# Kernel optimization log

Hardware: AMD Instinct MI355X
Metric: run time of the kernel (lower is better)

## Reference

```python
import jax, jax.numpy as jnp
import numpy as np

N, V, E, C_IN, C_OUT = 4, 4096, 2048, 64, 64


def setup_inputs() -> dict:
    key = jax.random.key(0)
    k_x, k_h, k_th = jax.random.split(key, 3)
    x = jax.random.normal(k_x, (N, V, C_IN), dtype=jnp.float32)
    H = (jax.random.uniform(k_h, (N, V, E)) < 0.05).astype(jnp.float32)
    # guarantee every vertex and every hyperedge has degree >= 1 (code divides by degree)
    v_idx = jnp.arange(V)
    H = H.at[:, v_idx, v_idx % E].set(1.0)
    # xavier_uniform for theta
    limit = float(np.sqrt(6.0 / (C_IN + C_OUT)))
    theta = jax.random.uniform(k_th, (C_IN, C_OUT), minval=-limit, maxval=limit, dtype=jnp.float32)
    bias = jnp.zeros((C_OUT,), dtype=jnp.float32)
    return {"x": x, "H": H, "theta": theta, "bias": bias}


def reference(x, H, theta, bias):
    # x: [N,V,C], H: [N,V,E] incidence, theta: [C,O], bias: [O]
    # Original builds diag_embed(1/deg) and multiplies; equivalent to direct
    # per-row / per-column scaling of H (same math, no NxVxV / NxExE diagonals).
    dv = 1.0 / H.sum(-1)            # [N,V] vertex degrees
    de = 1.0 / H.sum(1)             # [N,E] hyperedge degrees
    y = jnp.einsum('nvc,co->nvo', x, theta)          # [N,V,O]
    HDe = H * de[:, None, :]                          # H @ De  -> [N,V,E]
    y = jnp.einsum('nvc,nve->nec', y, HDe)            # vertex -> edge  [N,E,O]
    HDv = H * dv[:, :, None]                          # Dv @ H -> [N,V,E]
    y = jnp.einsum('nec,nve->nvc', y, HDv)            # edge -> vertex  [N,V,O]
    return y + bias[None, None, :]
```

## Files before the change

kernel.cpp:

```cpp
#include <hip/hip_runtime.h>
#include <hip/hip_bf16.h>
#include <stdint.h>

#define N_B 4
#define NV 4096
#define NE 2048

typedef float    f32x4  __attribute__((ext_vector_type(4)));
typedef __bf16   bf16x8 __attribute__((ext_vector_type(8)));
typedef unsigned short u16;
typedef u16      u16x8  __attribute__((ext_vector_type(8)));
typedef uint32_t u32x4  __attribute__((ext_vector_type(4)));

__device__ __forceinline__ u16 f2bf_rne(float f) {
    uint32_t u = __builtin_bit_cast(uint32_t, f);
    u += 0x7FFFu + ((u >> 16) & 1u);
    return (u16)(u >> 16);
}
__device__ __forceinline__ float bf2f(u16 h) {
    uint32_t u = ((uint32_t)h) << 16;
    return __builtin_bit_cast(float, u);
}
__device__ __forceinline__ f32x4 mfma_bf16(u16x8 a, u16x8 b, f32x4 c) {
    return __builtin_amdgcn_mfma_f32_16x16x32_bf16(
        __builtin_bit_cast(bf16x8, a), __builtin_bit_cast(bf16x8, b), c, 0, 0, 0);
}
__device__ __forceinline__ u16x8 expand8(uint32_t byte) {
    u32x4 w;
#pragma unroll
    for (int p = 0; p < 4; ++p) {
        const uint32_t lo = (byte >> (2 * p)) & 1u;
        const uint32_t hi = (byte >> (2 * p + 1)) & 1u;
        w[p] = (lo | (hi << 16)) * 0x3F80u;
    }
    return __builtin_bit_cast(u16x8, w);
}

__global__ __launch_bounds__(256) void k_pack(const float* __restrict__ H,
                                              uint32_t* __restrict__ HB,
                                              uint32_t* __restrict__ HT) {
    __shared__ float tile[64][65];
    const int bid = blockIdx.x;
    const int ex = bid & 31, vy = (bid >> 5) & 63, n = bid >> 11;
    const int e0 = ex * 64, v0 = vy * 64;
    const int t = threadIdx.x;
    const float* __restrict__ Hn = H + ((size_t)n * NV + v0) * NE + e0;

#pragma unroll
    for (int i = 0; i < 4; ++i) {
        const int idx = i * 256 + t;
        const int row = idx >> 4;
        const int q = (idx & 15) * 4;
        const float4 hv = *(const float4*)(Hn + (size_t)row * NE + q);
        tile[row][q] = hv.x; tile[row][q + 1] = hv.y;
        tile[row][q + 2] = hv.z; tile[row][q + 3] = hv.w;
    }
    __syncthreads();

    if (t < 128) {
        const int v = t >> 1, we = t & 1;
        uint32_t u = 0;
#pragma unroll
        for (int j = 0; j < 32; ++j)
            u |= (tile[v][we * 32 + j] != 0.0f) ? (1u << j) : 0u;
        HB[(((size_t)n * (NV / 16) + ((v0 + v) >> 4)) * (NE / 32) + (e0 >> 5) + we) * 16 +
           ((v0 + v) & 15)] = u;
    } else {
        const int e = (t - 128) >> 1, wv = t & 1;
        uint32_t u = 0;
#pragma unroll
        for (int j = 0; j < 32; ++j)
            u |= (tile[wv * 32 + j][e] != 0.0f) ? (1u << j) : 0u;
        HT[(((size_t)n * (NE / 16) + ((e0 + e) >> 4)) * (NV / 32) + (v0 >> 5) + wv) * 16 +
           ((e0 + e) & 15)] = u;
    }
}

__global__ __launch_bounds__(256) void k_xtheta(const float* __restrict__ x,
                                                const float* __restrict__ th,
                                                u16* __restrict__ Yh,
                                                u16* __restrict__ Yl) {
    __shared__ float xs[64][65];
    __shared__ float ts[64][65];
    const int t = threadIdx.x;
    const int n  = blockIdx.x >> 6;
    const int v0 = (blockIdx.x & 63) * 64;

#pragma unroll
    for (int i = 0; i < 4; ++i) {
        const int idx = i * 256 + t;
        const int row = idx >> 4, q = (idx & 15) * 4;
        const float4 xv = *(const float4*)&x[((size_t)(n * NV + v0 + row)) * 64 + q];
        const float4 tv = *(const float4*)&th[(size_t)row * 64 + q];
        xs[row][q] = xv.x; xs[row][q + 1] = xv.y; xs[row][q + 2] = xv.z; xs[row][q + 3] = xv.w;
        ts[row][q] = tv.x; ts[row][q + 1] = tv.y; ts[row][q + 2] = tv.z; ts[row][q + 3] = tv.w;
    }
    __syncthreads();

    const int v4 = (t & 15) * 4;
    const int c4 = (t >> 4) * 4;
    float acc[4][4] = {};
#pragma unroll
    for (int k = 0; k < 64; ++k) {
        float tv[4], xv[4];
#pragma unroll
        for (int i = 0; i < 4; ++i) { tv[i] = ts[k][c4 + i]; xv[i] = xs[v4 + i][k]; }
#pragma unroll
        for (int i = 0; i < 4; ++i)
#pragma unroll
            for (int j = 0; j < 4; ++j) acc[i][j] += tv[i] * xv[j];
    }
#pragma unroll
    for (int i = 0; i < 4; ++i) {
        ushort4 hi, lo;
        u16 h;
        h = f2bf_rne(acc[i][0]); hi.x = h; lo.x = f2bf_rne(acc[i][0] - bf2f(h));
        h = f2bf_rne(acc[i][1]); hi.y = h; lo.y = f2bf_rne(acc[i][1] - bf2f(h));
        h = f2bf_rne(acc[i][2]); hi.z = h; lo.z = f2bf_rne(acc[i][2] - bf2f(h));
        h = f2bf_rne(acc[i][3]); hi.w = h; lo.w = f2bf_rne(acc[i][3] - bf2f(h));
        const size_t o = ((size_t)n * 64 + c4 + i) * NV + v0 + v4;
        *(ushort4*)&Yh[o] = hi;
        *(ushort4*)&Yl[o] = lo;
    }
}

__global__ __launch_bounds__(256, 8) void k_v2e(const uint32_t* __restrict__ HT,
                                                const uint32_t* __restrict__ HB,
                                                const u16* __restrict__ Yh,
                                                const u16* __restrict__ Yl,
                                                float* __restrict__ P2,
                                                float* __restrict__ de,
                                                float* __restrict__ dv) {
    const int t = threadIdx.x;
    const int s2 = gridDim.y;
    const int lin = blockIdx.x + 32 * (blockIdx.y + s2 * blockIdx.z);
    const int nb = 32 * s2 * N_B;

    if (t < 64) {
        const int total = N_B * NE + N_B * NV;
        for (int id = lin * 64 + t; id < total; id += nb * 64) {
            if (id < N_B * NE) {
                const int n_ = id >> 11, e = id & (NE - 1);
                const uint32_t* p =
                    HT + ((size_t)n_ * (NE / 16) + (e >> 4)) * ((NV / 32) * 16) + (e & 15);
                uint32_t s = 0;
#pragma unroll 4
                for (int wv = 0; wv < NV / 32; ++wv) s += __popc(p[(size_t)wv * 16]);
                de[id] = (float)s;
            } else {
                const int j = id - N_B * NE;
                const int n_ = j >> 12, v = j & (NV - 1);
                const uint32_t* p =
                    HB + ((size_t)n_ * (NV / 16) + (v >> 4)) * ((NE / 32) * 16) + (v & 15);
                uint32_t s = 0;
#pragma unroll 4
                for (int we = 0; we < NE / 32; ++we) s += __popc(p[(size_t)we * 16]);
                dv[j] = (float)s;
            }
        }
    }

    const int wid = (lin & 7) * (nb >> 3) + (lin >> 3);
    const int n   = wid / (32 * s2);
    const int rem = wid % (32 * s2);
    const int sp  = rem >> 5;
    const int e0  = (rem & 31) * 64;

    const int krange = NV / s2;
    const int kk0 = sp * krange;
    const int S   = krange / 32;

    const int w = t >> 6, l = t & 63;
    const int lq = l >> 4, lr = l & 15;
    const int sh = lq * 8;
    const int hstride = (NV / 32) * 16;

    const uint32_t* __restrict__ ht =
        HT + ((size_t)n * (NE / 16) + (e0 >> 4)) * hstride + (kk0 >> 5) * 16 + lr;
    const u16* __restrict__ ybh = Yh + ((size_t)n * 64 + w * 16 + lr) * NV + kk0 + lq * 8;
    const u16* __restrict__ ybl = Yl + ((size_t)n * 64 + w * 16 + lr) * NV + kk0 + lq * 8;

    f32x4 acc0 = {0.f,0.f,0.f,0.f}, acc1 = acc0, acc2 = acc0, acc3 = acc0;

    uint32_t A[2][4];
#pragma unroll
    for (int d = 0; d < 2; ++d) {
        A[d][0] = ht[0 * hstride + d * 16];
        A[d][1] = ht[1 * hstride + d * 16];
        A[d][2] = ht[2 * hstride + d * 16];
        A[d][3] = ht[3 * hstride + d * 16];
    }
    u16x8 BH[2], BL[2];
    BH[0] = *(const u16x8*)ybh;
    BL[0] = *(const u16x8*)ybl;

#define V2E_STEP(s, u, GA, GB)                                                \
    {                                                                         \
        const uint32_t a0 = A[u][0], a1 = A[u][1], a2 = A[u][2], a3 = A[u][3];\
        if (GA) {                                                             \
            A[u][0] = ht[0 * hstride + ((s) + 2) * 16];                       \
            A[u][1] = ht[1 * hstride + ((s) + 2) * 16];                       \
            A[u][2] = ht[2 * hstride + ((s) + 2) * 16];                       \
            A[u][3] = ht[3 * hstride + ((s) + 2) * 16];                       \
        }                                                                     \
        if (GB) {                                                             \
            BH[((u) + 1) & 1] = *(const u16x8*)(ybh + ((s) + 1) * 32);        \
            BL[((u) + 1) & 1] = *(const u16x8*)(ybl + ((s) + 1) * 32);        \
        }                                                                     \
        const u16x8 bh = BH[u], bl = BL[u];                                   \
        u16x8 a;                                                              \
        a = expand8((a0 >> sh) & 0xFF);                                       \
        acc0 = mfma_bf16(a, bh, acc0); acc0 = mfma_bf16(a, bl, acc0);         \
        a = expand8((a1 >> sh) & 0xFF);                                       \
        acc1 = mfma_bf16(a, bh, acc1); acc1 = mfma_bf16(a, bl, acc1);         \
        a = expand8((a2 >> sh) & 0xFF);                                       \
        acc2 = mfma_bf16(a, bh, acc2); acc2 = mfma_bf16(a, bl, acc2);         \
        a = expand8((a3 >> sh) & 0xFF);                                       \
        acc3 = mfma_bf16(a, bh, acc3); acc3 = mfma_bf16(a, bl, acc3);         \
    }

    int sb = 0;
    for (; sb < S - 2; sb += 2) {
        V2E_STEP(sb + 0, 0, true, true)
        V2E_STEP(sb + 1, 1, true, true)
    }
    V2E_STEP(sb + 0, 0, false, true)
    V2E_STEP(sb + 1, 1, false, false)
#undef V2E_STEP

    float* pb = P2 + (((size_t)sp * N_B + n) * 64 + w * 16 + lr) * NE + e0 + lq * 4;
    *(f32x4*)(pb + 0)  = acc0;
    *(f32x4*)(pb + 16) = acc1;
    *(f32x4*)(pb + 32) = acc2;
    *(f32x4*)(pb + 48) = acc3;
}

__global__ __launch_bounds__(256) void k_red2(const float* __restrict__ P2,
                                              const float* __restrict__ de,
                                              u16* __restrict__ Zh,
                                              u16* __restrict__ Zl, int nsp) {
    const int i = blockIdx.x * 256 + threadIdx.x;
    const int row = i >> 9;
    const int e4  = (i & 511) * 4;
    const int n   = row >> 6;

    float4 a = make_float4(0.f, 0.f, 0.f, 0.f);
    for (int sp = 0; sp < nsp; ++sp) {
        const float4 p = *(const float4*)&P2[((size_t)sp * 256 + row) * NE + e4];
        a.x += p.x; a.y += p.y; a.z += p.z; a.w += p.w;
    }
    const float4 d = *(const float4*)&de[(size_t)n * NE + e4];
    float z[4] = {a.x / d.x, a.y / d.y, a.z / d.z, a.w / d.w};
    ushort4 hi, lo;
    u16 h;
    h = f2bf_rne(z[0]); hi.x = h; lo.x = f2bf_rne(z[0] - bf2f(h));
    h = f2bf_rne(z[1]); hi.y = h; lo.y = f2bf_rne(z[1] - bf2f(h));
    h = f2bf_rne(z[2]); hi.z = h; lo.z = f2bf_rne(z[2] - bf2f(h));
    h = f2bf_rne(z[3]); hi.w = h; lo.w = f2bf_rne(z[3] - bf2f(h));
    *(ushort4*)&Zh[(size_t)row * NE + e4] = hi;
    *(ushort4*)&Zl[(size_t)row * NE + e4] = lo;
}

__global__ __launch_bounds__(256, 8) void k_e2v(const uint32_t* __restrict__ HB,
                                                const u16* __restrict__ Zh,
                                                const u16* __restrict__ Zl,
                                                float* __restrict__ P3) {
    const int t = threadIdx.x;
    const int s3 = gridDim.y;
    const int lin = blockIdx.x + 64 * (blockIdx.y + s3 * blockIdx.z);
    const int nb = 64 * s3 * N_B;

    const int wid = (lin & 7) * (nb >> 3) + (lin >> 3);
    const int n   = wid / (64 * s3);
    const int rem = wid % (64 * s3);
    const int sp  = rem >> 6;
    const int v0  = (rem & 63) * 64;

    const int krange = NE / s3;
    const int kk0 = sp * krange;
    const int S   = krange / 32;

    const int w = t >> 6, l = t & 63;
    const int lq = l >> 4, lr = l & 15;
    const int sh = lq * 8;
    const int estride = (NE / 32) * 16;

    const uint32_t* __restrict__ hb =
        HB + ((size_t)n * (NV / 16) + (v0 >> 4)) * estride + (kk0 >> 5) * 16 + lr;
    const u16* __restrict__ zbh = Zh + ((size_t)n * 64 + w * 16 + lr) * NE + kk0 + lq * 8;
    const u16* __restrict__ zbl = Zl + ((size_t)n * 64 + w * 16 + lr) * NE + kk0 + lq * 8;

    f32x4 acc0 = {0.f,0.f,0.f,0.f}, acc1 = acc0, acc2 = acc0, acc3 = acc0;

    uint32_t A[2][4];
#pragma unroll
    for (int d = 0; d < 2; ++d) {
        A[d][0] = hb[0 * estride + d * 16];
        A[d][1] = hb[1 * estride + d * 16];
        A[d][2] = hb[2 * estride + d * 16];
        A[d][3] = hb[3 * estride + d * 16];
    }
    u16x8 BH[2], BL[2];
    BH[0] = *(const u16x8*)zbh;
    BL[0] = *(const u16x8*)zbl;

#define E2V_STEP(s, u, GA, GB)                                                \
    {                                                                         \
        const uint32_t a0 = A[u][0], a1 = A[u][1], a2 = A[u][2], a3 = A[u][3];\
        if (GA) {                                                             \
            A[u][0] = hb[0 * estride + ((s) + 2) * 16];                       \
            A[u][1] = hb[1 * estride + ((s) + 2) * 16];                       \
            A[u][2] = hb[2 * estride + ((s) + 2) * 16];                       \
            A[u][3] = hb[3 * estride + ((s) + 2) * 16];                       \
        }                                                                     \
        if (GB) {                                                             \
            BH[((u) + 1) & 1] = *(const u16x8*)(zbh + ((s) + 1) * 32);        \
            BL[((u) + 1) & 1] = *(const u16x8*)(zbl + ((s) + 1) * 32);        \
        }                                                                     \
        const u16x8 bh = BH[u], bl = BL[u];                                   \
        u16x8 a;                                                              \
        a = expand8((a0 >> sh) & 0xFF);                                       \
        acc0 = mfma_bf16(a, bh, acc0); acc0 = mfma_bf16(a, bl, acc0);         \
        a = expand8((a1 >> sh) & 0xFF);                                       \
        acc1 = mfma_bf16(a, bh, acc1); acc1 = mfma_bf16(a, bl, acc1);         \
        a = expand8((a2 >> sh) & 0xFF);                                       \
        acc2 = mfma_bf16(a, bh, acc2); acc2 = mfma_bf16(a, bl, acc2);         \
        a = expand8((a3 >> sh) & 0xFF);                                       \
        acc3 = mfma_bf16(a, bh, acc3); acc3 = mfma_bf16(a, bl, acc3);         \
    }

    int sb = 0;
    for (; sb < S - 2; sb += 2) {
        E2V_STEP(sb + 0, 0, true, true)
        E2V_STEP(sb + 1, 1, true, true)
    }
    E2V_STEP(sb + 0, 0, false, true)
    E2V_STEP(sb + 1, 1, false, false)
#undef E2V_STEP

    float* pb = P3 + (((size_t)sp * N_B + n) * 64 + w * 16 + lr) * NV + v0 + lq * 4;
    *(f32x4*)(pb + 0)  = acc0;
    *(f32x4*)(pb + 16) = acc1;
    *(f32x4*)(pb + 32) = acc2;
    *(f32x4*)(pb + 48) = acc3;
}

__global__ __launch_bounds__(512) void k_red3(const float* __restrict__ P3,
                                              const float* __restrict__ dv,
                                              const float* __restrict__ bias,
                                              float* __restrict__ out, int nsp) {
    __shared__ float lt[64][68];
    const int n  = blockIdx.y;
    const int v0 = blockIdx.x * 64;
    const int t  = threadIdx.x;

    {
        const int c   = t >> 3;
        const int vch = (t & 7) * 8;
        float4 s0 = make_float4(0.f, 0.f, 0.f, 0.f), s1 = s0;
        for (int sp = 0; sp < nsp; ++sp) {
            const size_t base = (((size_t)sp * N_B + n) * 64 + c) * NV + v0 + vch;
            const float4 p0 = *(const float4*)&P3[base];
            const float4 p1 = *(const float4*)&P3[base + 4];
            s0.x += p0.x; s0.y += p0.y; s0.z += p0.z; s0.w += p0.w;
            s1.x += p1.x; s1.y += p1.y; s1.z += p1.z; s1.w += p1.w;
        }
        *(float4*)&lt[c][vch]     = s0;
        *(float4*)&lt[c][vch + 4] = s1;
    }
    const int vw  = t >> 3;
    const int cch = (t & 7) * 8;
    const float dsum = dv[(size_t)n * NV + v0 + vw];
    __syncthreads();

    const float rdv = 1.0f / dsum;
    const float4 b0 = *(const float4*)&bias[cch];
    const float4 b1 = *(const float4*)&bias[cch + 4];
    float4 o0, o1;
    o0.x = lt[cch + 0][vw] * rdv + b0.x;
    o0.y = lt[cch + 1][vw] * rdv + b0.y;
    o0.z = lt[cch + 2][vw] * rdv + b0.z;
    o0.w = lt[cch + 3][vw] * rdv + b0.w;
    o1.x = lt[cch + 4][vw] * rdv + b1.x;
    o1.y = lt[cch + 5][vw] * rdv + b1.y;
    o1.z = lt[cch + 6][vw] * rdv + b1.z;
    o1.w = lt[cch + 7][vw] * rdv + b1.w;
    float* dst = out + ((size_t)n * NV + v0 + vw) * 64 + cch;
    *(float4*)dst       = o0;
    *(float4*)(dst + 4) = o1;
}

extern "C" void kernel_launch(void* const* d_in, const int* in_sizes, int n_in,
                              void* d_out, int out_size, void* d_ws, size_t ws_size,
                              hipStream_t stream) {
    const float* x     = (const float*)d_in[0];
    const float* H     = (const float*)d_in[1];
    const float* theta = (const float*)d_in[2];
    const float* bias  = (const float*)d_in[3];
    float* out = (float*)d_out;

    const size_t yE  = (size_t)N_B * 64 * NV;
    const size_t zE  = (size_t)N_B * 64 * NE;
    const size_t HBW = (size_t)N_B * (NV / 16) * (NE / 32) * 16;
    const size_t HTW = (size_t)N_B * (NE / 16) * (NV / 32) * 16;
    const size_t deE = (size_t)N_B * NE;
    const size_t dvE = (size_t)N_B * NV;

    u16* Yh = (u16*)d_ws;
    u16* Yl = Yh + yE;
    u16* Zh = Yl + yE;
    u16* Zl = Zh + zE;
    uint32_t* HB = (uint32_t*)(Zl + zE);
    uint32_t* HT = HB + HBW;
    float* de = (float*)(HT + HTW);
    float* dv = de + deE;
    float* fbase = dv + dvE;

    const size_t fixed_bytes = (size_t)((char*)fbase - (char*)d_ws);
    const size_t avail_f = (ws_size > fixed_bytes) ? (ws_size - fixed_bytes) / 4 : 0;

    int s2 = 2, s3 = 1;
    if      (avail_f >= 16 * zE + 8 * yE) { s2 = 16; s3 = 8; }
    else if (avail_f >=  8 * zE + 4 * yE) { s2 = 8;  s3 = 4; }
    else if (avail_f >=  4 * zE + 2 * yE) { s2 = 4;  s3 = 2; }

    float* P2 = fbase;
    float* P3 = P2 + (size_t)s2 * zE;

    k_pack<<<dim3(8192), 256, 0, stream>>>(H, HB, HT);
    k_xtheta<<<dim3(N_B * NV / 64), 256, 0, stream>>>(x, theta, Yh, Yl);
    k_v2e<<<dim3(NE / 64, s2, N_B), 256, 0, stream>>>(HT, HB, Yh, Yl, P2, de, dv);
    k_red2<<<dim3((int)(zE / 4 / 256)), 256, 0, stream>>>(P2, de, Zh, Zl, s2);
    k_e2v<<<dim3(NV / 64, s3, N_B), 256, 0, stream>>>(HB, Zh, Zl, P3);
    k_red3<<<dim3(NV / 64, N_B), 512, 0, stream>>>(P3, dv, bias, out, s3);
}
```

Before: 97.55 us.

## Split H packing into streaming bit-pack and bitwise transpose kernels

The single packing kernel, which staged float tiles of H in shared memory and built both row and column bitmasks, is split in two. The first kernel streams H directly, with each thread reading 32 contiguous floats and emitting one row bitmask word. The second transposes those packed bitmask words through a small shared-memory buffer to build the column-major bitmask. This removes the 64x65 float shared-memory tile and the strided column reads of it. In exchange it adds an extra kernel launch and a small re-read of the packed data, and each thread's per-row float4 reads are strided across lanes.

```diff
diff --git a/kernel.cpp b/kernel.cpp
--- a/kernel.cpp
+++ b/kernel.cpp
@@ -36,44 +36,50 @@
     return __builtin_bit_cast(u16x8, w);
 }
 
-__global__ __launch_bounds__(256) void k_pack(const float* __restrict__ H,
-                                              uint32_t* __restrict__ HB,
-                                              uint32_t* __restrict__ HT) {
-    __shared__ float tile[64][65];
+__global__ __launch_bounds__(256) void k_packB(const float* __restrict__ H,
+                                               uint32_t* __restrict__ HB) {
+    const int g = blockIdx.x * 256 + threadIdx.x;
+    const int r  = g >> 6;
+    const int wi = g & 63;
+    const int n  = r >> 12;
+    const int v  = r & (NV - 1);
+    const float* __restrict__ src = H + (size_t)r * NE + wi * 32;
+    uint32_t u = 0;
+#pragma unroll
+    for (int k = 0; k < 8; ++k) {
+        const float4 f = *(const float4*)(src + k * 4);
+        u |= (f.x != 0.f ? 1u : 0u) << (4 * k + 0);
+        u |= (f.y != 0.f ? 1u : 0u) << (4 * k + 1);
+        u |= (f.z != 0.f ? 1u : 0u) << (4 * k + 2);
+        u |= (f.w != 0.f ? 1u : 0u) << (4 * k + 3);
+    }
+    HB[(((size_t)n * (NV / 16) + (v >> 4)) * (NE / 32) + wi) * 16 + (v & 15)] = u;
+}
+
+__global__ __launch_bounds__(128) void k_packT(const uint32_t* __restrict__ HB,
+                                               uint32_t* __restrict__ HT) {
+    __shared__ uint32_t lds[2][64];
     const int bid = blockIdx.x;
     const int ex = bid & 31, vy = (bid >> 5) & 63, n = bid >> 11;
     const int e0 = ex * 64, v0 = vy * 64;
     const int t = threadIdx.x;
-    const float* __restrict__ Hn = H + ((size_t)n * NV + v0) * NE + e0;
-
-#pragma unroll
-    for (int i = 0; i < 4; ++i) {
-        const int idx = i * 256 + t;
-        const int row = idx >> 4;
-        const int q = (idx & 15) * 4;
-        const float4 hv = *(const float4*)(Hn + (size_t)row * NE + q);
-        tile[row][q] = hv.x; tile[row][q + 1] = hv.y;
-        tile[row][q + 2] = hv.z; tile[row][q + 3] = hv.w;
+
+    {
+        const int we = t >> 6, vl = t & 63;
+        lds[we][vl] =
+            HB[(((size_t)n * (NV / 16) + ((v0 + vl) >> 4)) * (NE / 32) + (e0 >> 5) + we) * 16 +
+               ((v0 + vl) & 15)];
     }
     __syncthreads();
 
-    if (t < 128) {
-        const int v = t >> 1, we = t & 1;
-        uint32_t u = 0;
-#pragma unroll
-        for (int j = 0; j < 32; ++j)
-            u |= (tile[v][we * 32 + j] != 0.0f) ? (1u << j) : 0u;
-        HB[(((size_t)n * (NV / 16) + ((v0 + v) >> 4)) * (NE / 32) + (e0 >> 5) + we) * 16 +
-           ((v0 + v) & 15)] = u;
-    } else {
-        const int e = (t - 128) >> 1, wv = t & 1;
-        uint32_t u = 0;
-#pragma unroll
-        for (int j = 0; j < 32; ++j)
-            u |= (tile[wv * 32 + j][e] != 0.0f) ? (1u << j) : 0u;
-        HT[(((size_t)n * (NE / 16) + ((e0 + e) >> 4)) * (NV / 32) + (v0 >> 5) + wv) * 16 +
-           ((e0 + e) & 15)] = u;
-    }
+    const int el = t >> 1, wv = t & 1;
+    const int wei = el >> 5, bit = el & 31;
+    uint32_t u = 0;
+#pragma unroll
+    for (int j = 0; j < 32; ++j)
+        u |= ((lds[wei][wv * 32 + j] >> bit) & 1u) << j;
+    HT[(((size_t)n * (NE / 16) + ((e0 + el) >> 4)) * (NV / 32) + (v0 >> 5) + wv) * 16 +
+       ((e0 + el) & 15)] = u;
 }
 
 __global__ __launch_bounds__(256) void k_xtheta(const float* __restrict__ x,
@@ -427,7 +433,8 @@
     float* P2 = fbase;
     float* P3 = P2 + (size_t)s2 * zE;
 
-    k_pack<<<dim3(8192), 256, 0, stream>>>(H, HB, HT);
+    k_packB<<<dim3(4096), 256, 0, stream>>>(H, HB);
+    k_packT<<<dim3(8192), 128, 0, stream>>>(HB, HT);
     k_xtheta<<<dim3(N_B * NV / 64), 256, 0, stream>>>(x, theta, Yh, Yl);
     k_v2e<<<dim3(NE / 64, s2, N_B), 256, 0, stream>>>(HT, HB, Yh, Yl, P2, de, dv);
     k_red2<<<dim3((int)(zE / 4 / 256)), 256, 0, stream>>>(P2, de, Zh, Zl, s2);
```

After: 105.1 us. 1.08x slower.
